# Kernel tuning notes

Measured on AMD Instinct MI355X. Metric: run time of the kernel, lower is better.

The kernel has to match this reference:

```python
import jax, jax.numpy as jnp
import numpy as np

N = 20000      # nodes
E = 320000     # edges
H = 128        # hidden_channels
F = 128        # num_filters
R = 50         # num_rbf
L = 6          # num_interactions
CU = 5.0       # cutoff_upper (cutoff_lower = 0)
ZMAX = 100


def cosine_cutoff(d):
    return 0.5 * (jnp.cos(d * jnp.pi / CU) + 1.0) * (d < CU).astype(d.dtype)


def expnorm_rbf(d, means, betas):
    # d: [E] -> [E, R]
    de = d[:, None]
    return cosine_cutoff(de) * jnp.exp(-betas * (jnp.exp(-de) - means) ** 2)


def setup_inputs() -> dict:
    key = jax.random.key(0)
    ks = jax.random.split(key, 24)
    s = 0.05
    inp = {
        "z": jax.random.randint(ks[0], (N,), 0, ZMAX),
        "edge_index": jax.random.randint(ks[1], (2, E), 0, N),
        "edge_weight": jax.random.uniform(ks[2], (E,), jnp.float32) * CU,
        # embedding + rbf params
        "emb": jax.random.normal(ks[3], (ZMAX, H), jnp.float32) * s,
        "means": jnp.linspace(np.exp(-CU), 1.0, R).astype(jnp.float32),
        "betas": jnp.full((R,), (2.0 / R * (1.0 - np.exp(-CU))) ** -2, jnp.float32),
        # neighbor embedding params (Linear stored as [in, out])
        "dp_w": jax.random.normal(ks[4], (R, H), jnp.float32) * s,
        "dp_b": jnp.zeros((H,), jnp.float32),
        "comb_w": jax.random.normal(ks[5], (2 * H, H), jnp.float32) * s,
        "comb_b": jnp.zeros((H,), jnp.float32),
        # per-layer interaction params, stacked over L
        "mlp_w1": jax.random.normal(ks[6], (L, R, F), jnp.float32) * s,
        "mlp_b1": jnp.zeros((L, F), jnp.float32),
        "mlp_w2": jax.random.normal(ks[7], (L, F, F), jnp.float32) * s,
        "mlp_b2": jnp.zeros((L, F), jnp.float32),
        "lin1_w": jax.random.normal(ks[8], (L, H, F), jnp.float32) * s,  # no bias
        "lin2_w": jax.random.normal(ks[9], (L, F, H), jnp.float32) * s,
        "lin2_b": jnp.zeros((L, H), jnp.float32),
        "lin_w": jax.random.normal(ks[10], (L, H, H), jnp.float32) * s,
        "lin_b": jnp.zeros((L, H), jnp.float32),
    }
    return inp


def reference(z, edge_index, edge_weight, emb, means, betas, dp_w, dp_b,
              comb_w, comb_b, mlp_w1, mlp_b1, mlp_w2, mlp_b2,
              lin1_w, lin2_w, lin2_b, lin_w, lin_b):
    j = edge_index[0]  # source (x_j gathered here)
    i = edge_index[1]  # target (aggregation index)

    C = cosine_cutoff(edge_weight)                 # [E]
    attr = expnorm_rbf(edge_weight, means, betas)  # [E, R]

    x = emb[z]                                     # [N, H]

    # --- NeighborEmbedding (aggr='add') ---
    Wn = (attr @ dp_w + dp_b) * C[:, None]         # [E, H]
    agg = jax.ops.segment_sum(x[j] * Wn, i, num_segments=N)
    x = jnp.concatenate([x, agg], axis=1) @ comb_w + comb_b

    # mean-aggregation denominator (PyG mean: 0 for isolated nodes)
    cnt = jax.ops.segment_sum(jnp.ones((E,), x.dtype), i, num_segments=N)
    inv_cnt = jnp.where(cnt > 0, 1.0 / jnp.maximum(cnt, 1.0), 0.0)[:, None]

    # --- Interaction blocks with residual ---
    for l in range(L):
        W = jax.nn.silu(attr @ mlp_w1[l] + mlp_b1[l]) @ mlp_w2[l] + mlp_b2[l]
        W = W * C[:, None]                         # [E, F]
        h = x @ lin1_w[l]                          # [N, F]
        h = jax.ops.segment_sum(h[j] * W, i, num_segments=N) * inv_cnt
        h = h @ lin2_w[l] + lin2_b[l]
        h = jax.nn.silu(h)
        h = h @ lin_w[l] + lin_b[l]
        x = x + h
    return x
```

## Files before the change

### kernel.cpp

```cpp
#include <hip/hip_runtime.h>
#include <hip/hip_bf16.h>
#include <math.h>

#define N_NODES 20000
#define N_EDGES 320000
#define NTILES  5000
#define HD 128
#define RD 50
#define NL 6
#define CUTV 5.0f
#define PI_F 3.14159265358979323846f
#define WPAD 132

typedef __attribute__((ext_vector_type(8))) short short8;
typedef __attribute__((ext_vector_type(4))) float f32x4;

__device__ __forceinline__ float cutoff_f(float d) {
  float c = 0.5f * (__cosf(d * (PI_F / CUTV)) + 1.0f);
  return d < CUTV ? c : 0.0f;
}
__device__ __forceinline__ float silu_f(float x) {
  return x / (1.0f + __expf(-x));
}
__device__ __forceinline__ unsigned short bf16bits(float f) {
  union { __hip_bfloat16 b; unsigned short u; } cv;
  cv.b = __float2bfloat16(f);
  return cv.u;
}
__device__ __forceinline__ float bfu_hi(unsigned int bits_in_high) {
  union { unsigned int u; float f; } v; v.u = bits_in_high; return v.f;
}
__device__ __forceinline__ f32x4 mfma16(short8 a, short8 b, f32x4 c) {
  return __builtin_amdgcn_mfma_f32_16x16x32_bf16(a, b, c, 0, 0, 0);
}
__device__ __forceinline__ void split8(const float* __restrict__ p,
                                       short8& h, short8& l) {
  float4 v0 = *(const float4*)p;
  float4 v1 = *(const float4*)(p + 4);
  float vv[8] = {v0.x, v0.y, v0.z, v0.w, v1.x, v1.y, v1.z, v1.w};
  #pragma unroll
  for (int i = 0; i < 8; ++i) {
    unsigned short hb = bf16bits(vv[i]);
    h[i] = (short)hb;
    l[i] = (short)bf16bits(vv[i] - bfu_hi((unsigned int)hb << 16));
  }
}

__global__ void k_hist(const int* __restrict__ ei, int* __restrict__ deg) {
  int e = blockIdx.x * blockDim.x + threadIdx.x;
  if (e < N_EDGES) atomicAdd(&deg[ei[N_EDGES + e]], 1);
}

__global__ void k_scan(const int* __restrict__ deg, int* __restrict__ rowptr,
                       int* __restrict__ cursor) {
  __shared__ int s[1024];
  __shared__ int run;
  int t = threadIdx.x;
  if (t == 0) run = 0;
  __syncthreads();
  for (int base = 0; base < N_NODES; base += 1024) {
    int idx = base + t;
    int v = (idx < N_NODES) ? deg[idx] : 0;
    s[t] = v;
    __syncthreads();
    for (int off = 1; off < 1024; off <<= 1) {
      int add = (t >= off) ? s[t - off] : 0;
      __syncthreads();
      s[t] += add;
      __syncthreads();
    }
    int excl = s[t] - v;
    int r = run;
    if (idx < N_NODES) { rowptr[idx] = r + excl; cursor[idx] = r + excl; }
    __syncthreads();
    if (t == 0) run += s[1023];
    __syncthreads();
  }
  if (t == 0) rowptr[N_NODES] = run;
}

__global__ void k_scatter(const int* __restrict__ ei, int* __restrict__ cursor,
                          int* __restrict__ eids) {
  int e = blockIdx.x * blockDim.x + threadIdx.x;
  if (e < N_EDGES) {
    int i = ei[N_EDGES + e];
    int p = atomicAdd(&cursor[i], 1);
    eids[p] = e;
  }
}

__global__ void k_init(const int* __restrict__ z, const float* __restrict__ emb,
                       float* __restrict__ x) {
  int idx = blockIdx.x * blockDim.x + threadIdx.x;
  if (idx < N_NODES * 32) {
    int n = idx >> 5, c4 = idx & 31;
    float4 v = ((const float4*)emb)[z[n] * 32 + c4];
    ((float4*)x)[n * 32 + c4] = v;
  }
}

__global__ __launch_bounds__(256)
void k_attr(const int* __restrict__ ei, const float* __restrict__ ew,
            const int* __restrict__ eids, const int* __restrict__ rowptr,
            const float* __restrict__ means, const float* __restrict__ betas,
            unsigned short* __restrict__ attr_fr, float* __restrict__ Csrt,
            float* __restrict__ Cinv, int* __restrict__ srcj) {
  int gid = blockIdx.x * blockDim.x + threadIdx.x;
  int tile = gid >> 9, s = gid & 511;
  int kg = s >> 6, e = s & 63;
  int p = tile * 64 + e;
  int eo = eids[p];
  float d = ew[eo];
  float C = cutoff_f(d);
  float ex = __expf(-d);
  short8 out;
  #pragma unroll
  for (int i = 0; i < 8; ++i) {
    int k = kg * 8 + i;
    float v = 0.0f;
    if (k < RD) {
      float em = ex - means[k];
      v = C * __expf(-betas[k] * em * em);
    }
    out[i] = (short)bf16bits(v);
  }
  *(short8*)(attr_fr + (size_t)gid * 8) = out;
  if (kg == 0) {
    Csrt[p] = C;
    srcj[p] = ei[eo];
    int dn = ei[N_EDGES + eo];
    int dg = rowptr[dn + 1] - rowptr[dn];
    Cinv[p] = C / (float)(dg > 0 ? dg : 1);
  }
}

template <bool TWO>
__global__ __launch_bounds__(256, 4)
void k_filter(const unsigned short* __restrict__ afr_g,
              const float* __restrict__ scale_e,
              const float* __restrict__ w1g, const float* __restrict__ b1g,
              const float* __restrict__ w2g, const float* __restrict__ bFg,
              unsigned short* __restrict__ Wout) {
  __shared__ unsigned short s_u[64 * WPAD];
  int t = threadIdx.x;
  int wv = t >> 6, lane = t & 63;
  int c = lane & 15, g = lane >> 4;

  short8 B1[2][2];
  #pragma unroll
  for (int ntl = 0; ntl < 2; ++ntl) {
    int col = (2 * wv + ntl) * 16 + c;
    #pragma unroll
    for (int kt = 0; kt < 2; ++kt) {
      short8 v;
      #pragma unroll
      for (int i = 0; i < 8; ++i) {
        int k = 32 * kt + 8 * g + i;
        v[i] = (k < RD) ? (short)bf16bits(w1g[k * HD + col]) : (short)0;
      }
      B1[ntl][kt] = v;
    }
  }
  short8 B2[2][4];
  if (TWO) {
    #pragma unroll
    for (int ntl = 0; ntl < 2; ++ntl) {
      int col = (2 * wv + ntl) * 16 + c;
      #pragma unroll
      for (int kt = 0; kt < 4; ++kt) {
        short8 v;
        #pragma unroll
        for (int i = 0; i < 8; ++i) {
          int k = 32 * kt + 8 * g + i;
          v[i] = (short)bf16bits(w2g[k * HD + col]);
        }
        B2[ntl][kt] = v;
      }
    }
  }
  float b1v[2], bFv[2];
  #pragma unroll
  for (int ntl = 0; ntl < 2; ++ntl) {
    int col = (2 * wv + ntl) * 16 + c;
    b1v[ntl] = TWO ? b1g[col] : 0.0f;
    bFv[ntl] = bFg[col];
  }

  for (int tile = blockIdx.x; tile < NTILES; tile += gridDim.x) {
    const unsigned short* afr = afr_g + (size_t)tile * 4096;
    f32x4 acc[4][2];
    #pragma unroll
    for (int mt = 0; mt < 4; ++mt) {
      acc[mt][0] = (f32x4){0.f, 0.f, 0.f, 0.f};
      acc[mt][1] = (f32x4){0.f, 0.f, 0.f, 0.f};
    }
    #pragma unroll
    for (int kt = 0; kt < 2; ++kt) {
      #pragma unroll
      for (int mt = 0; mt < 4; ++mt) {
        short8 a = *(const short8*)(afr + ((size_t)((4 * kt + g) * 64 + (16 * mt + c))) * 8);
        acc[mt][0] = mfma16(a, B1[0][kt], acc[mt][0]);
        acc[mt][1] = mfma16(a, B1[1][kt], acc[mt][1]);
      }
    }
    if (TWO) {
      #pragma unroll
      for (int mt = 0; mt < 4; ++mt) {
        #pragma unroll
        for (int ntl = 0; ntl < 2; ++ntl) {
          int ch = (2 * wv + ntl) * 16 + c;
          #pragma unroll
          for (int r = 0; r < 4; ++r) {
            int e = 16 * mt + 4 * g + r;
            float v = silu_f(acc[mt][ntl][r] + b1v[ntl]);
            s_u[((ch >> 3) * 64 + e) * 8 + (ch & 7)] = bf16bits(v);
          }
        }
      }
      __syncthreads();
      #pragma unroll
      for (int mt = 0; mt < 4; ++mt) {
        acc[mt][0] = (f32x4){0.f, 0.f, 0.f, 0.f};
        acc[mt][1] = (f32x4){0.f, 0.f, 0.f, 0.f};
      }
      #pragma unroll
      for (int kt = 0; kt < 4; ++kt) {
        #pragma unroll
        for (int mt = 0; mt < 4; ++mt) {
          short8 a = *(const short8*)(s_u + ((4 * kt + g) * 64 + (16 * mt + c)) * 8);
          acc[mt][0] = mfma16(a, B2[0][kt], acc[mt][0]);
          acc[mt][1] = mfma16(a, B2[1][kt], acc[mt][1]);
        }
      }
      __syncthreads();
    }
    #pragma unroll
    for (int mt = 0; mt < 4; ++mt) {
      float Cv[4];
      #pragma unroll
      for (int r = 0; r < 4; ++r) Cv[r] = scale_e[tile * 64 + 16 * mt + 4 * g + r];
      #pragma unroll
      for (int ntl = 0; ntl < 2; ++ntl) {
        int ch = (2 * wv + ntl) * 16 + c;
        #pragma unroll
        for (int r = 0; r < 4; ++r) {
          int e = 16 * mt + 4 * g + r;
          float v = (acc[mt][ntl][r] + bFv[ntl]) * Cv[r];
          s_u[e * WPAD + ch] = bf16bits(v);
        }
      }
    }
    __syncthreads();
    {
      short8* dst = (short8*)(Wout + (size_t)tile * 8192);
      #pragma unroll
      for (int k2 = 0; k2 < 4; ++k2) {
        int m = t + 256 * k2;
        int e = m >> 4, chunk = m & 15;
        dst[m] = *(const short8*)(s_u + e * WPAD + chunk * 8);
      }
    }
    __syncthreads();
  }
}

__global__ __launch_bounds__(256)
void k_segsum(const unsigned short* __restrict__ Wst, const float* __restrict__ h,
              const int* __restrict__ rowptr, const int* __restrict__ srcj,
              float* __restrict__ out) {
  int t = threadIdx.x, wv = t >> 6, lane = t & 63;
  int n = blockIdx.x * 4 + wv;
  if (n >= N_NODES) return;
  int half = lane >> 5;
  int q = lane & 31;
  int beg = rowptr[n], end = rowptr[n + 1];
  float a0 = 0.f, a1 = 0.f, a2 = 0.f, a3 = 0.f;
  #pragma unroll 4
  for (int p = beg + half; p < end; p += 2) {
    int j = srcj[p];
    uint2 wb = *(const uint2*)(Wst + (size_t)p * 128 + 4 * q);
    float4 hv = *(const float4*)(h + (size_t)j * 128 + 4 * q);
    a0 += hv.x * bfu_hi(wb.x << 16);
    a1 += hv.y * bfu_hi(wb.x & 0xffff0000u);
    a2 += hv.z * bfu_hi(wb.y << 16);
    a3 += hv.w * bfu_hi(wb.y & 0xffff0000u);
  }
  a0 += __shfl_xor(a0, 32, 64);
  a1 += __shfl_xor(a1, 32, 64);
  a2 += __shfl_xor(a2, 32, 64);
  a3 += __shfl_xor(a3, 32, 64);
  if (half == 0) {
    *(float4*)(out + (size_t)n * 128 + 4 * q) = make_float4(a0, a1, a2, a3);
  }
}

template <int KT, bool HASB, bool SILU, bool ADD>
__global__ __launch_bounds__(512)
void k_nmfma(const float* __restrict__ in1, const float* __restrict__ in2,
             const float* __restrict__ Wg, const float* __restrict__ bias,
             float* __restrict__ out) {
  int t = threadIdx.x;
  int wv = t >> 6, lane = t & 63;
  int c = lane & 15, g = lane >> 4;
  int col = 16 * wv + c;
  int n0 = blockIdx.x * 32;

  short8 Bh[KT], Bl[KT];
  #pragma unroll
  for (int kt = 0; kt < KT; ++kt) {
    short8 h, l;
    #pragma unroll
    for (int i = 0; i < 8; ++i) {
      int k = 32 * kt + 8 * g + i;
      float w = Wg[(size_t)k * HD + col];
      unsigned short hb = bf16bits(w);
      h[i] = (short)hb;
      l[i] = (short)bf16bits(w - bfu_hi((unsigned int)hb << 16));
    }
    Bh[kt] = h; Bl[kt] = l;
  }

  f32x4 acc[2];
  acc[0] = (f32x4){0.f, 0.f, 0.f, 0.f};
  acc[1] = (f32x4){0.f, 0.f, 0.f, 0.f};

  #pragma unroll
  for (int kt = 0; kt < KT; ++kt) {
    const float* in = (KT == 8 && kt >= 4) ? in2 : in1;
    int koff = (kt & 3) * 32 + 8 * g;
    #pragma unroll
    for (int mt = 0; mt < 2; ++mt) {
      int row = n0 + 16 * mt + c;
      int rowc = row < N_NODES ? row : N_NODES - 1;
      short8 ah, al;
      split8(in + (size_t)rowc * HD + koff, ah, al);
      acc[mt] = mfma16(ah, Bh[kt], acc[mt]);
      acc[mt] = mfma16(al, Bh[kt], acc[mt]);
      acc[mt] = mfma16(ah, Bl[kt], acc[mt]);
    }
  }
  __syncthreads();
  float bv = HASB ? bias[col] : 0.0f;
  #pragma unroll
  for (int mt = 0; mt < 2; ++mt) {
    #pragma unroll
    for (int r = 0; r < 4; ++r) {
      int row = n0 + 16 * mt + 4 * g + r;
      if (row < N_NODES) {
        float v = acc[mt][r] + bv;
        if (SILU) v = silu_f(v);
        if (ADD) out[(size_t)row * HD + col] += v;
        else out[(size_t)row * HD + col] = v;
      }
    }
  }
}

__global__ __launch_bounds__(512)
void k_nmfma2(const float* __restrict__ in1,
              const float* __restrict__ W1, const float* __restrict__ b1,
              const float* __restrict__ W2, const float* __restrict__ b2,
              float* __restrict__ xout) {
  __shared__ unsigned short s_uh[4096];
  __shared__ unsigned short s_ul[4096];
  int t = threadIdx.x;
  int wv = t >> 6, lane = t & 63;
  int c = lane & 15, g = lane >> 4;
  int col = 16 * wv + c;
  int n0 = blockIdx.x * 32;

  short8 B1h[4], B1l[4], B2h[4], B2l[4];
  #pragma unroll
  for (int kt = 0; kt < 4; ++kt) {
    short8 h1, l1, h2, l2;
    #pragma unroll
    for (int i = 0; i < 8; ++i) {
      int k = 32 * kt + 8 * g + i;
      float w = W1[(size_t)k * HD + col];
      unsigned short hb = bf16bits(w);
      h1[i] = (short)hb;
      l1[i] = (short)bf16bits(w - bfu_hi((unsigned int)hb << 16));
      float w2 = W2[(size_t)k * HD + col];
      unsigned short hb2 = bf16bits(w2);
      h2[i] = (short)hb2;
      l2[i] = (short)bf16bits(w2 - bfu_hi((unsigned int)hb2 << 16));
    }
    B1h[kt] = h1; B1l[kt] = l1; B2h[kt] = h2; B2l[kt] = l2;
  }
  float b1v = b1[col], b2v = b2[col];

  f32x4 acc[2];
  acc[0] = (f32x4){0.f, 0.f, 0.f, 0.f};
  acc[1] = (f32x4){0.f, 0.f, 0.f, 0.f};
  #pragma unroll
  for (int kt = 0; kt < 4; ++kt) {
    int koff = kt * 32 + 8 * g;
    #pragma unroll
    for (int mt = 0; mt < 2; ++mt) {
      int row = n0 + 16 * mt + c;
      int rowc = row < N_NODES ? row : N_NODES - 1;
      short8 ah, al;
      split8(in1 + (size_t)rowc * HD + koff, ah, al);
      acc[mt] = mfma16(ah, B1h[kt], acc[mt]);
      acc[mt] = mfma16(al, B1h[kt], acc[mt]);
      acc[mt] = mfma16(ah, B1l[kt], acc[mt]);
    }
  }
  #pragma unroll
  for (int mt = 0; mt < 2; ++mt) {
    #pragma unroll
    for (int r = 0; r < 4; ++r) {
      int e = 16 * mt + 4 * g + r;
      float v = silu_f(acc[mt][r] + b1v);
      unsigned short hb = bf16bits(v);
      unsigned short lb = bf16bits(v - bfu_hi((unsigned int)hb << 16));
      int idx = ((col >> 3) * 32 + e) * 8 + (col & 7);
      s_uh[idx] = hb;
      s_ul[idx] = lb;
    }
  }
  __syncthreads();
  acc[0] = (f32x4){0.f, 0.f, 0.f, 0.f};
  acc[1] = (f32x4){0.f, 0.f, 0.f, 0.f};
  #pragma unroll
  for (int kt = 0; kt < 4; ++kt) {
    #pragma unroll
    for (int mt = 0; mt < 2; ++mt) {
      int idx = ((4 * kt + g) * 32 + (16 * mt + c)) * 8;
      short8 ah = *(const short8*)(s_uh + idx);
      short8 al = *(const short8*)(s_ul + idx);
      acc[mt] = mfma16(ah, B2h[kt], acc[mt]);
      acc[mt] = mfma16(al, B2h[kt], acc[mt]);
      acc[mt] = mfma16(ah, B2l[kt], acc[mt]);
    }
  }
  #pragma unroll
  for (int mt = 0; mt < 2; ++mt) {
    #pragma unroll
    for (int r = 0; r < 4; ++r) {
      int row = n0 + 16 * mt + 4 * g + r;
      if (row < N_NODES) {
        xout[(size_t)row * HD + col] += acc[mt][r] + b2v;
      }
    }
  }
}

extern "C" void kernel_launch(void* const* d_in, const int* in_sizes, int n_in,
                              void* d_out, int out_size, void* d_ws, size_t ws_size,
                              hipStream_t stream) {
  const int* z = (const int*)d_in[0];
  const int* ei = (const int*)d_in[1];
  const float* ew = (const float*)d_in[2];
  const float* emb = (const float*)d_in[3];
  const float* means = (const float*)d_in[4];
  const float* betas = (const float*)d_in[5];
  const float* dp_w = (const float*)d_in[6];
  const float* dp_b = (const float*)d_in[7];
  const float* comb_w = (const float*)d_in[8];
  const float* comb_b = (const float*)d_in[9];
  const float* mlp_w1 = (const float*)d_in[10];
  const float* mlp_b1 = (const float*)d_in[11];
  const float* mlp_w2 = (const float*)d_in[12];
  const float* mlp_b2 = (const float*)d_in[13];
  const float* lin1_w = (const float*)d_in[14];
  const float* lin2_w = (const float*)d_in[15];
  const float* lin2_b = (const float*)d_in[16];
  const float* lin_w = (const float*)d_in[17];
  const float* lin_b = (const float*)d_in[18];
  float* x = (float*)d_out;

  int* rowptr = (int*)d_ws;
  int* deg = rowptr + 20032;
  int* cursor = deg + 20032;
  int* eids = cursor + 20032;
  int* srcj = eids + N_EDGES;
  float* Csrt = (float*)(srcj + N_EDGES);
  float* Cinv = Csrt + N_EDGES;
  unsigned short* attr_fr = (unsigned short*)(Cinv + N_EDGES);
  unsigned short* Wst = attr_fr + (size_t)N_EDGES * 64;
  float* hbuf = (float*)(Wst + (size_t)N_EDGES * 128);
  float* aggb = hbuf + (size_t)N_NODES * HD;

  hipMemsetAsync(deg, 0, N_NODES * sizeof(int), stream);
  k_hist<<<(N_EDGES + 255) / 256, 256, 0, stream>>>(ei, deg);
  k_scan<<<1, 1024, 0, stream>>>(deg, rowptr, cursor);
  k_scatter<<<(N_EDGES + 255) / 256, 256, 0, stream>>>(ei, cursor, eids);
  k_attr<<<NTILES * 2, 256, 0, stream>>>(ei, ew, eids, rowptr, means, betas,
                                         attr_fr, Csrt, Cinv, srcj);
  k_init<<<(N_NODES * 32 + 255) / 256, 256, 0, stream>>>(z, emb, x);

  k_filter<false><<<2500, 256, 0, stream>>>(attr_fr, Csrt, dp_w, nullptr,
                                            nullptr, dp_b, Wst);
  k_segsum<<<5000, 256, 0, stream>>>(Wst, x, rowptr, srcj, aggb);
  k_nmfma<8, true, false, false><<<625, 512, 0, stream>>>(x, aggb, comb_w,
                                                          comb_b, x);

  for (int l = 0; l < NL; ++l) {
    k_nmfma<4, false, false, false><<<625, 512, 0, stream>>>(
        x, nullptr, lin1_w + (size_t)l * HD * HD, nullptr, hbuf);
    k_filter<true><<<2500, 256, 0, stream>>>(
        attr_fr, Cinv,
        mlp_w1 + (size_t)l * RD * HD, mlp_b1 + (size_t)l * HD,
        mlp_w2 + (size_t)l * HD * HD, mlp_b2 + (size_t)l * HD, Wst);
    k_segsum<<<5000, 256, 0, stream>>>(Wst, hbuf, rowptr, srcj, aggb);
    k_nmfma2<<<625, 512, 0, stream>>>(
        aggb, lin2_w + (size_t)l * HD * HD, lin2_b + (size_t)l * HD,
        lin_w + (size_t)l * HD * HD, lin_b + (size_t)l * HD, x);
  }
}
```

Baseline: 896.0 us.

## Store filter output in MFMA fragment layout, read it directly in segsum

The filter kernel now writes its bf16 edge weights straight from the MFMA accumulator registers into global memory, packing pairs of edges per 32-bit word in a fragment-native layout. This removes the LDS staging transpose and two barriers per tile. The segment-sum kernel is rewritten to decode that layout, processing two consecutive edges per 16-byte load with bounds guards. Global stores become 4-byte scattered writes instead of 16-byte row-contiguous ones, and segsum does more index arithmetic and some wasted loads at segment boundaries.

```diff
diff --git a/kernel.cpp b/kernel.cpp
--- a/kernel.cpp
+++ b/kernel.cpp
@@ -10,7 +10,6 @@
 #define NL 6
 #define CUTV 5.0f
 #define PI_F 3.14159265358979323846f
-#define WPAD 132
 
 typedef __attribute__((ext_vector_type(8))) short short8;
 typedef __attribute__((ext_vector_type(4))) float f32x4;
@@ -140,8 +139,8 @@
               const float* __restrict__ scale_e,
               const float* __restrict__ w1g, const float* __restrict__ b1g,
               const float* __restrict__ w2g, const float* __restrict__ bFg,
-              unsigned short* __restrict__ Wout) {
-  __shared__ unsigned short s_u[64 * WPAD];
+              unsigned int* __restrict__ Wout) {
+  __shared__ unsigned short s_u[TWO ? 8192 : 8];
   int t = threadIdx.x;
   int wv = t >> 6, lane = t & 63;
   int c = lane & 15, g = lane >> 4;
@@ -204,6 +203,7 @@
       }
     }
     if (TWO) {
+      __syncthreads();
       #pragma unroll
       for (int mt = 0; mt < 4; ++mt) {
         #pragma unroll
@@ -232,8 +232,8 @@
           acc[mt][1] = mfma16(a, B2[1][kt], acc[mt][1]);
         }
       }
-      __syncthreads();
-    }
+    }
+    unsigned int* wt = Wout + (size_t)tile * 4096;
     #pragma unroll
     for (int mt = 0; mt < 4; ++mt) {
       float Cv[4];
@@ -241,49 +241,54 @@
       for (int r = 0; r < 4; ++r) Cv[r] = scale_e[tile * 64 + 16 * mt + 4 * g + r];
       #pragma unroll
       for (int ntl = 0; ntl < 2; ++ntl) {
-        int ch = (2 * wv + ntl) * 16 + c;
         #pragma unroll
-        for (int r = 0; r < 4; ++r) {
-          int e = 16 * mt + 4 * g + r;
-          float v = (acc[mt][ntl][r] + bFv[ntl]) * Cv[r];
-          s_u[e * WPAD + ch] = bf16bits(v);
+        for (int rp = 0; rp < 2; ++rp) {
+          float vlo = (acc[mt][ntl][2 * rp] + bFv[ntl]) * Cv[2 * rp];
+          float vhi = (acc[mt][ntl][2 * rp + 1] + bFv[ntl]) * Cv[2 * rp + 1];
+          unsigned int pk = (unsigned int)bf16bits(vlo) |
+                            ((unsigned int)bf16bits(vhi) << 16);
+          wt[((mt * 2 + ntl) * 2 + rp) * 256 + t] = pk;
         }
       }
     }
-    __syncthreads();
-    {
-      short8* dst = (short8*)(Wout + (size_t)tile * 8192);
-      #pragma unroll
-      for (int k2 = 0; k2 < 4; ++k2) {
-        int m = t + 256 * k2;
-        int e = m >> 4, chunk = m & 15;
-        dst[m] = *(const short8*)(s_u + e * WPAD + chunk * 8);
-      }
-    }
-    __syncthreads();
   }
 }
 
 __global__ __launch_bounds__(256)
-void k_segsum(const unsigned short* __restrict__ Wst, const float* __restrict__ h,
+void k_segsum(const unsigned int* __restrict__ Wst, const float* __restrict__ h,
               const int* __restrict__ rowptr, const int* __restrict__ srcj,
               float* __restrict__ out) {
-  int t = threadIdx.x, wv = t >> 6, lane = t & 63;
-  int n = blockIdx.x * 4 + wv;
+  int t = threadIdx.x, wvv = t >> 6, lane = t & 63;
+  int n = blockIdx.x * 4 + wvv;
   if (n >= N_NODES) return;
   int half = lane >> 5;
   int q = lane & 31;
+  int A = (q >> 3) * 64 + ((4 * q) & 15);
+  int ntl = (q >> 2) & 1;
   int beg = rowptr[n], end = rowptr[n + 1];
   float a0 = 0.f, a1 = 0.f, a2 = 0.f, a3 = 0.f;
-  #pragma unroll 4
-  for (int p = beg + half; p < end; p += 2) {
-    int j = srcj[p];
-    uint2 wb = *(const uint2*)(Wst + (size_t)p * 128 + 4 * q);
-    float4 hv = *(const float4*)(h + (size_t)j * 128 + 4 * q);
-    a0 += hv.x * bfu_hi(wb.x << 16);
-    a1 += hv.y * bfu_hi(wb.x & 0xffff0000u);
-    a2 += hv.z * bfu_hi(wb.y << 16);
-    a3 += hv.w * bfu_hi(wb.y & 0xffff0000u);
+  #pragma unroll 2
+  for (int pe = (beg & ~1) + 2 * half; pe < end; pe += 4) {
+    int tile = pe >> 6, e = pe & 63;
+    int mt = e >> 4, gg = (e >> 2) & 3, rp = (e >> 1) & 1;
+    uint4 w4 = *(const uint4*)(Wst + (size_t)tile * 4096 +
+                               ((mt * 2 + ntl) * 2 + rp) * 256 + gg * 16 + A);
+    if (pe >= beg) {
+      int j0 = srcj[pe];
+      float4 h0 = *(const float4*)(h + (size_t)j0 * 128 + 4 * q);
+      a0 += h0.x * bfu_hi(w4.x << 16);
+      a1 += h0.y * bfu_hi(w4.y << 16);
+      a2 += h0.z * bfu_hi(w4.z << 16);
+      a3 += h0.w * bfu_hi(w4.w << 16);
+    }
+    if (pe + 1 < end) {
+      int j1 = srcj[pe + 1];
+      float4 h1 = *(const float4*)(h + (size_t)j1 * 128 + 4 * q);
+      a0 += h1.x * bfu_hi(w4.x & 0xffff0000u);
+      a1 += h1.y * bfu_hi(w4.y & 0xffff0000u);
+      a2 += h1.z * bfu_hi(w4.z & 0xffff0000u);
+      a3 += h1.w * bfu_hi(w4.w & 0xffff0000u);
+    }
   }
   a0 += __shfl_xor(a0, 32, 64);
   a1 += __shfl_xor(a1, 32, 64);
@@ -478,8 +483,8 @@
   float* Csrt = (float*)(srcj + N_EDGES);
   float* Cinv = Csrt + N_EDGES;
   unsigned short* attr_fr = (unsigned short*)(Cinv + N_EDGES);
-  unsigned short* Wst = attr_fr + (size_t)N_EDGES * 64;
-  float* hbuf = (float*)(Wst + (size_t)N_EDGES * 128);
+  unsigned int* Wst = (unsigned int*)(attr_fr + (size_t)N_EDGES * 64);
+  float* hbuf = (float*)(Wst + (size_t)N_EDGES * 64);
   float* aggb = hbuf + (size_t)N_NODES * HD;
 
   hipMemsetAsync(deg, 0, N_NODES * sizeof(int), stream);
```

Result: slower. 951.6 us (+6.2%).

## Pre-split weights into bf16 hi/lo once and parallelize CSR scan

Applied to the files above, without the earlier changes.

Adds a k_wsplit pre-pass that converts the fp32 weight matrices into transposed bf16 hi/lo arrays once per call. The node GEMM kernels then load ready-made short8 fragments instead of doing strided fp32 loads and splitting in every one of 625 blocks. It also replaces the single-block serial scan with a three-kernel block-sum, block-scan and scan-out over 79 blocks. The cost is a few extra small launches and extra workspace.

```diff
diff --git a/kernel.cpp b/kernel.cpp
--- a/kernel.cpp
+++ b/kernel.cpp
@@ -11,6 +11,7 @@
 #define CUTV 5.0f
 #define PI_F 3.14159265358979323846f
 #define WPAD 132
+#define SCAN_B 79
 
 typedef __attribute__((ext_vector_type(8))) short short8;
 typedef __attribute__((ext_vector_type(4))) float f32x4;
@@ -51,32 +52,47 @@
   if (e < N_EDGES) atomicAdd(&deg[ei[N_EDGES + e]], 1);
 }
 
-__global__ void k_scan(const int* __restrict__ deg, int* __restrict__ rowptr,
-                       int* __restrict__ cursor) {
-  __shared__ int s[1024];
-  __shared__ int run;
-  int t = threadIdx.x;
-  if (t == 0) run = 0;
+__global__ void k_bsum(const int* __restrict__ deg, int* __restrict__ bsum) {
+  __shared__ int sdata[256];
+  int b = blockIdx.x, t = threadIdx.x;
+  int i = b * 256 + t;
+  sdata[t] = (i < N_NODES) ? deg[i] : 0;
   __syncthreads();
-  for (int base = 0; base < N_NODES; base += 1024) {
-    int idx = base + t;
-    int v = (idx < N_NODES) ? deg[idx] : 0;
-    s[t] = v;
+  for (int off = 128; off > 0; off >>= 1) {
+    if (t < off) sdata[t] += sdata[t + off];
     __syncthreads();
-    for (int off = 1; off < 1024; off <<= 1) {
-      int add = (t >= off) ? s[t - off] : 0;
-      __syncthreads();
-      s[t] += add;
-      __syncthreads();
-    }
-    int excl = s[t] - v;
-    int r = run;
-    if (idx < N_NODES) { rowptr[idx] = r + excl; cursor[idx] = r + excl; }
+  }
+  if (t == 0) bsum[b] = sdata[0];
+}
+
+__global__ void k_bscan(const int* __restrict__ bsum, int* __restrict__ boff,
+                        int* __restrict__ rowptrN) {
+  if (threadIdx.x == 0) {
+    int run = 0;
+    for (int b = 0; b < SCAN_B; ++b) { boff[b] = run; run += bsum[b]; }
+    rowptrN[0] = run;
+  }
+}
+
+__global__ void k_scanout(const int* __restrict__ deg, const int* __restrict__ boff,
+                          int* __restrict__ rowptr, int* __restrict__ cursor) {
+  __shared__ int sdata[256];
+  int b = blockIdx.x, t = threadIdx.x;
+  int i = b * 256 + t;
+  int v = (i < N_NODES) ? deg[i] : 0;
+  sdata[t] = v;
+  __syncthreads();
+  for (int off = 1; off < 256; off <<= 1) {
+    int add = (t >= off) ? sdata[t - off] : 0;
     __syncthreads();
-    if (t == 0) run += s[1023];
+    sdata[t] += add;
     __syncthreads();
   }
-  if (t == 0) rowptr[N_NODES] = run;
+  if (i < N_NODES) {
+    int excl = boff[b] + sdata[t] - v;
+    rowptr[i] = excl;
+    cursor[i] = excl;
+  }
 }
 
 __global__ void k_scatter(const int* __restrict__ ei, int* __restrict__ cursor,
@@ -97,6 +113,20 @@
     float4 v = ((const float4*)emb)[z[n] * 32 + c4];
     ((float4*)x)[n * 32 + c4] = v;
   }
+}
+
+__global__ void k_wsplit(const float* __restrict__ src,
+                         unsigned short* __restrict__ hi,
+                         unsigned short* __restrict__ lo, int K, int L) {
+  int idx = blockIdx.x * blockDim.x + threadIdx.x;
+  if (idx >= L * K * 128) return;
+  int l = idx / (K * 128);
+  int r = idx - l * (K * 128);
+  int k = r >> 7, col = r & 127;
+  float w = src[idx];
+  unsigned short hb = bf16bits(w);
+  hi[(size_t)l * K * 128 + col * K + k] = hb;
+  lo[(size_t)l * K * 128 + col * K + k] = bf16bits(w - bfu_hi((unsigned int)hb << 16));
 }
 
 __global__ __launch_bounds__(256)
@@ -297,8 +327,9 @@
 template <int KT, bool HASB, bool SILU, bool ADD>
 __global__ __launch_bounds__(512)
 void k_nmfma(const float* __restrict__ in1, const float* __restrict__ in2,
-             const float* __restrict__ Wg, const float* __restrict__ bias,
-             float* __restrict__ out) {
+             const unsigned short* __restrict__ Wh,
+             const unsigned short* __restrict__ Wl,
+             const float* __restrict__ bias, float* __restrict__ out) {
   int t = threadIdx.x;
   int wv = t >> 6, lane = t & 63;
   int c = lane & 15, g = lane >> 4;
@@ -308,16 +339,8 @@
   short8 Bh[KT], Bl[KT];
   #pragma unroll
   for (int kt = 0; kt < KT; ++kt) {
-    short8 h, l;
-    #pragma unroll
-    for (int i = 0; i < 8; ++i) {
-      int k = 32 * kt + 8 * g + i;
-      float w = Wg[(size_t)k * HD + col];
-      unsigned short hb = bf16bits(w);
-      h[i] = (short)hb;
-      l[i] = (short)bf16bits(w - bfu_hi((unsigned int)hb << 16));
-    }
-    Bh[kt] = h; Bl[kt] = l;
+    Bh[kt] = *(const short8*)(Wh + (size_t)col * (KT * 32) + kt * 32 + 8 * g);
+    Bl[kt] = *(const short8*)(Wl + (size_t)col * (KT * 32) + kt * 32 + 8 * g);
   }
 
   f32x4 acc[2];
@@ -358,8 +381,11 @@
 
 __global__ __launch_bounds__(512)
 void k_nmfma2(const float* __restrict__ in1,
-              const float* __restrict__ W1, const float* __restrict__ b1,
-              const float* __restrict__ W2, const float* __restrict__ b2,
+              const unsigned short* __restrict__ W1h,
+              const unsigned short* __restrict__ W1l,
+              const unsigned short* __restrict__ W2h,
+              const unsigned short* __restrict__ W2l,
+              const float* __restrict__ b1, const float* __restrict__ b2,
               float* __restrict__ xout) {
   __shared__ unsigned short s_uh[4096];
   __shared__ unsigned short s_ul[4096];
@@ -372,20 +398,11 @@
   short8 B1h[4], B1l[4], B2h[4], B2l[4];
   #pragma unroll
   for (int kt = 0; kt < 4; ++kt) {
-    short8 h1, l1, h2, l2;
-    #pragma unroll
-    for (int i = 0; i < 8; ++i) {
-      int k = 32 * kt + 8 * g + i;
-      float w = W1[(size_t)k * HD + col];
-      unsigned short hb = bf16bits(w);
-      h1[i] = (short)hb;
-      l1[i] = (short)bf16bits(w - bfu_hi((unsigned int)hb << 16));
-      float w2 = W2[(size_t)k * HD + col];
-      unsigned short hb2 = bf16bits(w2);
-      h2[i] = (short)hb2;
-      l2[i] = (short)bf16bits(w2 - bfu_hi((unsigned int)hb2 << 16));
-    }
-    B1h[kt] = h1; B1l[kt] = l1; B2h[kt] = h2; B2l[kt] = l2;
+    size_t o = (size_t)col * 128 + kt * 32 + 8 * g;
+    B1h[kt] = *(const short8*)(W1h + o);
+    B1l[kt] = *(const short8*)(W1l + o);
+    B2h[kt] = *(const short8*)(W2h + o);
+    B2l[kt] = *(const short8*)(W2l + o);
   }
   float b1v = b1[col], b2v = b2[col];
 
@@ -473,7 +490,9 @@
   int* rowptr = (int*)d_ws;
   int* deg = rowptr + 20032;
   int* cursor = deg + 20032;
-  int* eids = cursor + 20032;
+  int* bsum = cursor + 20032;
+  int* boff = bsum + 128;
+  int* eids = boff + 128;
   int* srcj = eids + N_EDGES;
   float* Csrt = (float*)(srcj + N_EDGES);
   float* Cinv = Csrt + N_EDGES;
@@ -481,31 +500,47 @@
   unsigned short* Wst = attr_fr + (size_t)N_EDGES * 64;
   float* hbuf = (float*)(Wst + (size_t)N_EDGES * 128);
   float* aggb = hbuf + (size_t)N_NODES * HD;
+  unsigned short* combh = (unsigned short*)(aggb + (size_t)N_NODES * HD);
+  unsigned short* combl = combh + 32768;
+  unsigned short* l1h = combl + 32768;
+  unsigned short* l1l = l1h + 98304;
+  unsigned short* l2h = l1l + 98304;
+  unsigned short* l2l = l2h + 98304;
+  unsigned short* lnh = l2l + 98304;
+  unsigned short* lnl = lnh + 98304;
 
   hipMemsetAsync(deg, 0, N_NODES * sizeof(int), stream);
   k_hist<<<(N_EDGES + 255) / 256, 256, 0, stream>>>(ei, deg);
-  k_scan<<<1, 1024, 0, stream>>>(deg, rowptr, cursor);
+  k_bsum<<<SCAN_B, 256, 0, stream>>>(deg, bsum);
+  k_bscan<<<1, 64, 0, stream>>>(bsum, boff, rowptr + N_NODES);
+  k_scanout<<<SCAN_B, 256, 0, stream>>>(deg, boff, rowptr, cursor);
   k_scatter<<<(N_EDGES + 255) / 256, 256, 0, stream>>>(ei, cursor, eids);
   k_attr<<<NTILES * 2, 256, 0, stream>>>(ei, ew, eids, rowptr, means, betas,
                                          attr_fr, Csrt, Cinv, srcj);
   k_init<<<(N_NODES * 32 + 255) / 256, 256, 0, stream>>>(z, emb, x);
+  k_wsplit<<<(32768 + 255) / 256, 256, 0, stream>>>(comb_w, combh, combl, 256, 1);
+  k_wsplit<<<(98304 + 255) / 256, 256, 0, stream>>>(lin1_w, l1h, l1l, 128, 6);
+  k_wsplit<<<(98304 + 255) / 256, 256, 0, stream>>>(lin2_w, l2h, l2l, 128, 6);
+  k_wsplit<<<(98304 + 255) / 256, 256, 0, stream>>>(lin_w, lnh, lnl, 128, 6);
 
   k_filter<false><<<2500, 256, 0, stream>>>(attr_fr, Csrt, dp_w, nullptr,
                                             nullptr, dp_b, Wst);
   k_segsum<<<5000, 256, 0, stream>>>(Wst, x, rowptr, srcj, aggb);
-  k_nmfma<8, true, false, false><<<625, 512, 0, stream>>>(x, aggb, comb_w,
+  k_nmfma<8, true, false, false><<<625, 512, 0, stream>>>(x, aggb, combh, combl,
                                                           comb_b, x);
 
   for (int l = 0; l < NL; ++l) {
     k_nmfma<4, false, false, false><<<625, 512, 0, stream>>>(
-        x, nullptr, lin1_w + (size_t)l * HD * HD, nullptr, hbuf);
+        x, nullptr, l1h + (size_t)l * 16384, l1l + (size_t)l * 16384,
+        nullptr, hbuf);
     k_filter<true><<<2500, 256, 0, stream>>>(
         attr_fr, Cinv,
         mlp_w1 + (size_t)l * RD * HD, mlp_b1 + (size_t)l * HD,
         mlp_w2 + (size_t)l * HD * HD, mlp_b2 + (size_t)l * HD, Wst);
     k_segsum<<<5000, 256, 0, stream>>>(Wst, hbuf, rowptr, srcj, aggb);
     k_nmfma2<<<625, 512, 0, stream>>>(
-        aggb, lin2_w + (size_t)l * HD * HD, lin2_b + (size_t)l * HD,
-        lin_w + (size_t)l * HD * HD, lin_b + (size_t)l * HD, x);
-  }
-}
+        aggb, l2h + (size_t)l * 16384, l2l + (size_t)l * 16384,
+        lnh + (size_t)l * 16384, lnl + (size_t)l * 16384,
+        lin2_b + (size_t)l * HD, lin_b + (size_t)l * HD, x);
+  }
+}
```

New measurement: 936.8 us. 1.05x slower.
